# Optimization experiments

Measured on AMD Instinct MI355X. Metric: run time of the kernel, lower is better.

Reference implementation:

```python
import jax, jax.numpy as jnp
import numpy as np

EMBED = 1024
HEADS = 16
HEAD_DIM = EMBED // HEADS
MLP_HIDDEN = 4096


def _layernorm(x, g, b, eps=1e-5):
    mu = jnp.mean(x, axis=-1, keepdims=True)
    var = jnp.mean(jnp.square(x - mu), axis=-1, keepdims=True)
    return (x - mu) * jax.lax.rsqrt(var + eps) * g + b


def setup_inputs() -> dict:
    key = jax.random.key(0)
    ks = jax.random.split(key, 8)
    s = 0.02
    return {
        "x": jax.random.normal(ks[0], (8, 1024, EMBED), dtype=jnp.float32),
        "qkv_w": jax.random.normal(ks[1], (EMBED, 3 * EMBED), dtype=jnp.float32) * s,
        "qkv_b": jnp.zeros((3 * EMBED,), jnp.float32),
        "proj_w": jax.random.normal(ks[2], (EMBED, EMBED), dtype=jnp.float32) * s,
        "proj_b": jnp.zeros((EMBED,), jnp.float32),
        "fc1_w": jax.random.normal(ks[3], (EMBED, MLP_HIDDEN), dtype=jnp.float32) * s,
        "fc1_b": jnp.zeros((MLP_HIDDEN,), jnp.float32),
        "fc2_w": jax.random.normal(ks[4], (MLP_HIDDEN, EMBED), dtype=jnp.float32) * s,
        "fc2_b": jnp.zeros((EMBED,), jnp.float32),
        "ln1_g": jnp.ones((EMBED,), jnp.float32),
        "ln1_b": jnp.zeros((EMBED,), jnp.float32),
        "ln2_g": jnp.ones((EMBED,), jnp.float32),
        "ln2_b": jnp.zeros((EMBED,), jnp.float32),
    }


def reference(x, qkv_w, qkv_b, proj_w, proj_b, fc1_w, fc1_b, fc2_w, fc2_b,
              ln1_g, ln1_b, ln2_g, ln2_b):
    B, N, C = x.shape
    scale = HEAD_DIM ** -0.5

    # --- MHSA on pre-norm input ---
    h = _layernorm(x, ln1_g, ln1_b)
    qkv = h @ qkv_w + qkv_b                      # [B,N,3C]
    qkv = qkv.reshape(B, N, 3, HEADS, HEAD_DIM)
    q, k, v = (qkv[:, :, i].transpose(0, 2, 1, 3) for i in range(3))  # [B,H,N,d]
    attn = jnp.einsum('bhqd,bhkd->bhqk', q, k) * scale
    attn = jax.nn.softmax(attn, axis=-1)
    o = jnp.einsum('bhqk,bhkd->bhqd', attn, v)   # [B,H,N,d]
    o = o.transpose(0, 2, 1, 3).reshape(B, N, C)
    x = x + (o @ proj_w + proj_b)

    # --- MLP ---
    h2 = _layernorm(x, ln2_g, ln2_b)
    h2 = jax.nn.gelu(h2 @ fc1_w + fc1_b, approximate=False)
    x = x + (h2 @ fc2_w + fc2_b)
    return x
```

## Files before the change

### kernel.cpp

```cpp
#include <hip/hip_runtime.h>
#include <hip/hip_bf16.h>

typedef __bf16 bf16x8 __attribute__((ext_vector_type(8)));
typedef float  f32x4  __attribute__((ext_vector_type(4)));
typedef unsigned short u16;

static __device__ __forceinline__ u16 f2bf(float f) {
  union { float f; unsigned u; } v; v.f = f;
  unsigned r = v.u + 0x7fffu + ((v.u >> 16) & 1u);
  return (u16)(r >> 16);
}

static __device__ __forceinline__ void gld16(const void* g, void* l) {
  __builtin_amdgcn_global_load_lds(
      (const __attribute__((address_space(1))) unsigned int*)g,
      (__attribute__((address_space(3))) unsigned int*)l, 16, 0, 0);
}

#define SBAR() do { __builtin_amdgcn_sched_barrier(0); \
                    __builtin_amdgcn_s_barrier(); \
                    __builtin_amdgcn_sched_barrier(0); } while (0)

__global__ __launch_bounds__(256) void transpose_cast_k(
    const float* __restrict__ W, u16* __restrict__ Wt, int K, int N) {
  __shared__ float tile[32][33];
  const int t = threadIdx.x;
  const int n0 = blockIdx.x * 32, k0 = blockIdx.y * 32;
  const int r = t >> 3, c4 = (t & 7) * 4;
  const float4 v = *(const float4*)(W + (size_t)(k0 + r) * N + n0 + c4);
  tile[r][c4 + 0] = v.x; tile[r][c4 + 1] = v.y;
  tile[r][c4 + 2] = v.z; tile[r][c4 + 3] = v.w;
  __syncthreads();
  const int n = t >> 3, k4 = (t & 7) * 4;
  uint2 pk;
  pk.x = f2bf(tile[k4 + 0][n]) | ((unsigned)f2bf(tile[k4 + 1][n]) << 16);
  pk.y = f2bf(tile[k4 + 2][n]) | ((unsigned)f2bf(tile[k4 + 3][n]) << 16);
  *(uint2*)(Wt + (size_t)(n0 + n) * K + k0 + k4) = pk;
}

__global__ __launch_bounds__(256) void ln_cast_k(
    const float* __restrict__ x, const float* __restrict__ g,
    const float* __restrict__ b, u16* __restrict__ out) {
  __shared__ float red[2][4];
  const int t = threadIdx.x;
  const size_t row = blockIdx.x;
  const float4 v = *(const float4*)(x + row * 1024 + t * 4);
  float s = v.x + v.y + v.z + v.w;
  float ss = v.x * v.x + v.y * v.y + v.z * v.z + v.w * v.w;
  #pragma unroll
  for (int m = 1; m <= 32; m <<= 1) { s += __shfl_xor(s, m); ss += __shfl_xor(ss, m); }
  if ((t & 63) == 0) { red[0][t >> 6] = s; red[1][t >> 6] = ss; }
  __syncthreads();
  s  = red[0][0] + red[0][1] + red[0][2] + red[0][3];
  ss = red[1][0] + red[1][1] + red[1][2] + red[1][3];
  const float mu = s * (1.f / 1024.f);
  const float var = ss * (1.f / 1024.f) - mu * mu;
  const float rs = rsqrtf(var + 1e-5f);
  const float4 gv = *(const float4*)(g + t * 4);
  const float4 bv = *(const float4*)(b + t * 4);
  uint2 pk;
  pk.x = f2bf((v.x - mu) * rs * gv.x + bv.x) |
         ((unsigned)f2bf((v.y - mu) * rs * gv.y + bv.y) << 16);
  pk.y = f2bf((v.z - mu) * rs * gv.z + bv.z) |
         ((unsigned)f2bf((v.w - mu) * rs * gv.w + bv.w) << 16);
  *(uint2*)(out + row * 1024 + t * 4) = pk;
}

template <int EPI>
__global__ __launch_bounds__(512, 2) void gemm8_k(
    const u16* __restrict__ A, const u16* __restrict__ Bt,
    const float* __restrict__ bias, u16* __restrict__ Cb, float* __restrict__ Cf,
    const float* __restrict__ R, u16* __restrict__ vT, int M, int N, int K) {
  __shared__ u16 As[2][16384];
  __shared__ u16 Bs[2][16384];
  const int t = threadIdx.x;
  const int mt = M >> 8;
  const int tm = blockIdx.x % mt, tn = blockIdx.x / mt;
  const int lo = t & 15, hi = (t >> 4) & 3, wid = t >> 6;
  const int wm = wid >> 2, wn = wid & 3;
  const int NT = K >> 6;

  const int srow = t >> 3;
  const int sc = (t & 7) ^ (srow & 7);
  const u16* gA = A  + (size_t)(tm * 256) * K;
  const u16* gB = Bt + (size_t)(tn * 256) * K;
  auto stA = [&](int dd, int c, int T) {
    gld16(gA + (size_t)(c * 64 + srow) * K + (size_t)T * 64 + sc * 8,
          &As[dd][c * 4096 + t * 8]);
  };
  auto stB = [&](int dd, int c, int T) {
    gld16(gB + (size_t)(c * 64 + srow) * K + (size_t)T * 64 + sc * 8,
          &Bs[dd][c * 4096 + t * 8]);
  };

  const int xr = lo & 7;
  const int rowA = wm * 128 + lo;
  const int rowB = wn * 64 + lo;
#define RD_A(d, m, kk) (*(const bf16x8*)&As[d][(rowA + (m)*16)*64 + ((((kk)<<2)+hi)^xr)*8])
#define RD_B(d, n, kk) (*(const bf16x8*)&Bs[d][(rowB + (n)*16)*64 + ((((kk)<<2)+hi)^xr)*8])
#define MF(a, b, c) __builtin_amdgcn_mfma_f32_16x16x32_bf16(a, b, c, 0, 0, 0)

  f32x4 acc[8][4];
  #pragma unroll
  for (int i = 0; i < 8; ++i)
    #pragma unroll
    for (int j = 0; j < 4; ++j) acc[i][j] = (f32x4){0.f, 0.f, 0.f, 0.f};

  stA(0, 0, 0); stA(0, 1, 0); stA(0, 2, 0); stA(0, 3, 0);
  stB(0, 0, 0); stB(0, 1, 0); stB(0, 2, 0); stB(0, 3, 0);
  stB(1, 0, 1); stB(1, 1, 1); stB(1, 2, 1); stB(1, 3, 1);
  stA(1, 0, 1); stA(1, 2, 1);
  asm volatile("s_waitcnt vmcnt(6)" ::: "memory");
  SBAR();

  for (int T = 0; T < NT; ++T) {
    const int d = T & 1, dn = d ^ 1;
    bf16x8 b00 = RD_B(d,0,0), b01 = RD_B(d,0,1), b10 = RD_B(d,1,0), b11 = RD_B(d,1,1);
    bf16x8 b20 = RD_B(d,2,0), b21 = RD_B(d,2,1), b30 = RD_B(d,3,0), b31 = RD_B(d,3,1);
    bf16x8 a00 = RD_A(d,0,0), a01 = RD_A(d,0,1), a10 = RD_A(d,1,0), a11 = RD_A(d,1,1);
    if (T + 1 < NT) { stA(dn, 1, T + 1); stA(dn, 3, T + 1); }
    SBAR();
    __builtin_amdgcn_s_setprio(1);
    acc[0][0]=MF(a00,b00,acc[0][0]); acc[0][0]=MF(a01,b01,acc[0][0]);
    acc[0][1]=MF(a00,b10,acc[0][1]); acc[0][1]=MF(a01,b11,acc[0][1]);
    acc[0][2]=MF(a00,b20,acc[0][2]); acc[0][2]=MF(a01,b21,acc[0][2]);
    acc[0][3]=MF(a00,b30,acc[0][3]); acc[0][3]=MF(a01,b31,acc[0][3]);
    acc[1][0]=MF(a10,b00,acc[1][0]); acc[1][0]=MF(a11,b01,acc[1][0]);
    acc[1][1]=MF(a10,b10,acc[1][1]); acc[1][1]=MF(a11,b11,acc[1][1]);
    acc[1][2]=MF(a10,b20,acc[1][2]); acc[1][2]=MF(a11,b21,acc[1][2]);
    acc[1][3]=MF(a10,b30,acc[1][3]); acc[1][3]=MF(a11,b31,acc[1][3]);
    __builtin_amdgcn_s_setprio(0);
    SBAR();
    a00 = RD_A(d,2,0); a01 = RD_A(d,2,1); a10 = RD_A(d,3,0); a11 = RD_A(d,3,1);
    if (T + 2 < NT) { stB(d, 0, T + 2); stB(d, 1, T + 2); }
    SBAR();
    __builtin_amdgcn_s_setprio(1);
    acc[2][0]=MF(a00,b00,acc[2][0]); acc[2][0]=MF(a01,b01,acc[2][0]);
    acc[2][1]=MF(a00,b10,acc[2][1]); acc[2][1]=MF(a01,b11,acc[2][1]);
    acc[2][2]=MF(a00,b20,acc[2][2]); acc[2][2]=MF(a01,b21,acc[2][2]);
    acc[2][3]=MF(a00,b30,acc[2][3]); acc[2][3]=MF(a01,b31,acc[2][3]);
    acc[3][0]=MF(a10,b00,acc[3][0]); acc[3][0]=MF(a11,b01,acc[3][0]);
    acc[3][1]=MF(a10,b10,acc[3][1]); acc[3][1]=MF(a11,b11,acc[3][1]);
    acc[3][2]=MF(a10,b20,acc[3][2]); acc[3][2]=MF(a11,b21,acc[3][2]);
    acc[3][3]=MF(a10,b30,acc[3][3]); acc[3][3]=MF(a11,b31,acc[3][3]);
    __builtin_amdgcn_s_setprio(0);
    SBAR();
    a00 = RD_A(d,4,0); a01 = RD_A(d,4,1); a10 = RD_A(d,5,0); a11 = RD_A(d,5,1);
    if (T + 2 < NT) { stB(d, 2, T + 2); stB(d, 3, T + 2); }
    SBAR();
    __builtin_amdgcn_s_setprio(1);
    acc[4][0]=MF(a00,b00,acc[4][0]); acc[4][0]=MF(a01,b01,acc[4][0]);
    acc[4][1]=MF(a00,b10,acc[4][1]); acc[4][1]=MF(a01,b11,acc[4][1]);
    acc[4][2]=MF(a00,b20,acc[4][2]); acc[4][2]=MF(a01,b21,acc[4][2]);
    acc[4][3]=MF(a00,b30,acc[4][3]); acc[4][3]=MF(a01,b31,acc[4][3]);
    acc[5][0]=MF(a10,b00,acc[5][0]); acc[5][0]=MF(a11,b01,acc[5][0]);
    acc[5][1]=MF(a10,b10,acc[5][1]); acc[5][1]=MF(a11,b11,acc[5][1]);
    acc[5][2]=MF(a10,b20,acc[5][2]); acc[5][2]=MF(a11,b21,acc[5][2]);
    acc[5][3]=MF(a10,b30,acc[5][3]); acc[5][3]=MF(a11,b31,acc[5][3]);
    __builtin_amdgcn_s_setprio(0);
    SBAR();
    a00 = RD_A(d,6,0); a01 = RD_A(d,6,1); a10 = RD_A(d,7,0); a11 = RD_A(d,7,1);
    if (T + 2 < NT) { stA(d, 0, T + 2); stA(d, 2, T + 2); }
    SBAR();
    __builtin_amdgcn_s_setprio(1);
    acc[6][0]=MF(a00,b00,acc[6][0]); acc[6][0]=MF(a01,b01,acc[6][0]);
    acc[6][1]=MF(a00,b10,acc[6][1]); acc[6][1]=MF(a01,b11,acc[6][1]);
    acc[6][2]=MF(a00,b20,acc[6][2]); acc[6][2]=MF(a01,b21,acc[6][2]);
    acc[6][3]=MF(a00,b30,acc[6][3]); acc[6][3]=MF(a01,b31,acc[6][3]);
    acc[7][0]=MF(a10,b00,acc[7][0]); acc[7][0]=MF(a11,b01,acc[7][0]);
    acc[7][1]=MF(a10,b10,acc[7][1]); acc[7][1]=MF(a11,b11,acc[7][1]);
    acc[7][2]=MF(a10,b20,acc[7][2]); acc[7][2]=MF(a11,b21,acc[7][2]);
    acc[7][3]=MF(a10,b30,acc[7][3]); acc[7][3]=MF(a11,b31,acc[7][3]);
    __builtin_amdgcn_s_setprio(0);
    if (T < NT - 2)       { asm volatile("s_waitcnt vmcnt(6)" ::: "memory"); }
    else if (T == NT - 2) { asm volatile("s_waitcnt vmcnt(0)" ::: "memory"); }
    SBAR();
  }

  #pragma unroll
  for (int ni = 0; ni < 4; ++ni) {
    const int col = tn * 256 + wn * 64 + ni * 16 + lo;
    const float bv = bias[col];
    #pragma unroll
    for (int mi = 0; mi < 8; ++mi) {
      const int row0 = tm * 256 + wm * 128 + mi * 16 + hi * 4;
      const f32x4 v = acc[mi][ni];
      float vals[4];
      #pragma unroll
      for (int r = 0; r < 4; ++r) {
        float val = v[r] + bv;
        if (EPI == 1) val = 0.5f * val * (1.f + erff(val * 0.70710678118f));
        vals[r] = val;
      }
      if (EPI == 2) {
        #pragma unroll
        for (int r = 0; r < 4; ++r) {
          const size_t idx = (size_t)(row0 + r) * N + col;
          Cf[idx] = vals[r] + R[idx];
        }
      } else {
        #pragma unroll
        for (int r = 0; r < 4; ++r)
          Cb[(size_t)(row0 + r) * N + col] = f2bf(vals[r]);
        if (EPI == 3 && col >= 2048) {
          const int bb = row0 >> 10, n = row0 & 1023;
          const int hh = (col - 2048) >> 6, dd = col & 63;
          uint2 pk;
          pk.x = f2bf(vals[0]) | ((unsigned)f2bf(vals[1]) << 16);
          pk.y = f2bf(vals[2]) | ((unsigned)f2bf(vals[3]) << 16);
          *(uint2*)(vT + ((size_t)((bb * 16 + hh) * 64 + dd) << 10) + n) = pk;
        }
      }
    }
  }
#undef RD_A
#undef RD_B
#undef MF
}

__global__ __launch_bounds__(256, 2) void attn_k(
    const u16* __restrict__ qkv, const u16* __restrict__ vT, u16* __restrict__ o) {
  __shared__ u16 lK[64 * 64];
  __shared__ u16 lV[64 * 64];
  __shared__ u16 lP[64 * 72];
  const int t = threadIdx.x;
  const int lo = t & 15, hi = (t >> 4) & 3, w = t >> 6;
  const int qt = blockIdx.x & 15, bh = blockIdx.x >> 4;
  const int b = bh >> 4, h = bh & 15;
  const int q0 = qt * 64;
  const u16* Qb = qkv + (size_t)b * 1024 * 3072 + h * 64;
  const u16* Kb = Qb + 1024;
  const u16* Vt = vT + (size_t)bh * 64 * 1024;

  bf16x8 qf[2];
  {
    const size_t q = q0 + w * 16 + lo;
    qf[0] = *(const bf16x8*)(Qb + q * 3072 + hi * 8);
    qf[1] = *(const bf16x8*)(Qb + q * 3072 + 32 + hi * 8);
  }
  f32x4 oacc[4];
  #pragma unroll
  for (int i = 0; i < 4; ++i) oacc[i] = (f32x4){0.f, 0.f, 0.f, 0.f};
  float m = -1e30f, lsum = 0.f;
  const int srow = t >> 3, scol = (t & 7) * 8;

  for (int kv0 = 0; kv0 < 1024; kv0 += 64) {
    __syncthreads();
    #pragma unroll
    for (int j = 0; j < 2; ++j) {
      const int row = j * 32 + srow;
      gld16(Kb + (size_t)(kv0 + row) * 3072 + scol, &lK[(j * 256 + t) * 8]);
      gld16(Vt + (size_t)row * 1024 + kv0 + scol, &lV[(j * 256 + t) * 8]);
    }
    __syncthreads();

    f32x4 s[4];
    #pragma unroll
    for (int i = 0; i < 4; ++i) s[i] = (f32x4){0.f, 0.f, 0.f, 0.f};
    #pragma unroll
    for (int kk = 0; kk < 2; ++kk) {
      #pragma unroll
      for (int mi = 0; mi < 4; ++mi) {
        const bf16x8 kf = *(const bf16x8*)&lK[(mi * 16 + lo) * 64 + kk * 32 + hi * 8];
        s[mi] = __builtin_amdgcn_mfma_f32_16x16x32_bf16(kf, qf[kk], s[mi], 0, 0, 0);
      }
    }
    float sv[16];
    float tmax = -1e30f;
    #pragma unroll
    for (int mi = 0; mi < 4; ++mi)
      #pragma unroll
      for (int r = 0; r < 4; ++r) {
        const float xx = s[mi][r] * 0.125f;
        sv[mi * 4 + r] = xx;
        tmax = fmaxf(tmax, xx);
      }
    tmax = fmaxf(tmax, __shfl_xor(tmax, 16));
    tmax = fmaxf(tmax, __shfl_xor(tmax, 32));
    const float mnew = fmaxf(m, tmax);
    const float alpha = __expf(m - mnew);
    m = mnew;
    float p[16], ts = 0.f;
    #pragma unroll
    for (int i = 0; i < 16; ++i) { p[i] = __expf(sv[i] - mnew); ts += p[i]; }
    ts += __shfl_xor(ts, 16);
    ts += __shfl_xor(ts, 32);
    lsum = lsum * alpha + ts;
    #pragma unroll
    for (int mi = 0; mi < 4; ++mi) {
      uint2 pk;
      pk.x = f2bf(p[mi * 4 + 0]) | ((unsigned)f2bf(p[mi * 4 + 1]) << 16);
      pk.y = f2bf(p[mi * 4 + 2]) | ((unsigned)f2bf(p[mi * 4 + 3]) << 16);
      *(uint2*)&lP[(w * 16 + lo) * 72 + mi * 16 + hi * 4] = pk;
    }
    asm volatile("s_waitcnt lgkmcnt(0)" ::: "memory");
    float ar[4];
    #pragma unroll
    for (int r = 0; r < 4; ++r) ar[r] = __shfl(alpha, hi * 4 + r);
    #pragma unroll
    for (int ni = 0; ni < 4; ++ni)
      #pragma unroll
      for (int r = 0; r < 4; ++r) oacc[ni][r] *= ar[r];
    #pragma unroll
    for (int kk = 0; kk < 2; ++kk) {
      const bf16x8 pf = *(const bf16x8*)&lP[(w * 16 + lo) * 72 + kk * 32 + hi * 8];
      #pragma unroll
      for (int ni = 0; ni < 4; ++ni) {
        const bf16x8 vf = *(const bf16x8*)&lV[(ni * 16 + lo) * 64 + kk * 32 + hi * 8];
        oacc[ni] = __builtin_amdgcn_mfma_f32_16x16x32_bf16(pf, vf, oacc[ni], 0, 0, 0);
      }
    }
  }
  float lr[4];
  #pragma unroll
  for (int r = 0; r < 4; ++r) lr[r] = 1.f / __shfl(lsum, hi * 4 + r);
  #pragma unroll
  for (int ni = 0; ni < 4; ++ni) {
    const int d = ni * 16 + lo;
    #pragma unroll
    for (int r = 0; r < 4; ++r) {
      const int n = q0 + w * 16 + hi * 4 + r;
      o[((size_t)(b * 1024 + n) * 16 + h) * 64 + d] = f2bf(oacc[ni][r] * lr[r]);
    }
  }
}

extern "C" void kernel_launch(void* const* d_in, const int* in_sizes, int n_in,
                              void* d_out, int out_size, void* d_ws, size_t ws_size,
                              hipStream_t stream) {
  const float* x      = (const float*)d_in[0];
  const float* qkv_w  = (const float*)d_in[1];
  const float* qkv_b  = (const float*)d_in[2];
  const float* proj_w = (const float*)d_in[3];
  const float* proj_b = (const float*)d_in[4];
  const float* fc1_w  = (const float*)d_in[5];
  const float* fc1_b  = (const float*)d_in[6];
  const float* fc2_w  = (const float*)d_in[7];
  const float* fc2_b  = (const float*)d_in[8];
  const float* ln1_g  = (const float*)d_in[9];
  const float* ln1_b  = (const float*)d_in[10];
  const float* ln2_g  = (const float*)d_in[11];
  const float* ln2_b  = (const float*)d_in[12];
  float* out = (float*)d_out;
  char* ws = (char*)d_ws;
  u16* wqkvT = (u16*)(ws);
  u16* wprojT = (u16*)(ws + 6291456);
  u16* wfc1T = (u16*)(ws + 8388608);
  u16* wfc2T = (u16*)(ws + 16777216);
  u16* hbuf  = (u16*)(ws + 25165824);
  u16* qkvo  = (u16*)(ws + 41943040);
  u16* vT    = (u16*)(ws + 92274688);
  u16* fc1o  = qkvo;

  transpose_cast_k<<<dim3(96, 32),  256, 0, stream>>>(qkv_w,  wqkvT, 1024, 3072);
  transpose_cast_k<<<dim3(32, 32),  256, 0, stream>>>(proj_w, wprojT, 1024, 1024);
  transpose_cast_k<<<dim3(128, 32), 256, 0, stream>>>(fc1_w,  wfc1T, 1024, 4096);
  transpose_cast_k<<<dim3(32, 128), 256, 0, stream>>>(fc2_w,  wfc2T, 4096, 1024);
  ln_cast_k<<<8192, 256, 0, stream>>>(x, ln1_g, ln1_b, hbuf);
  gemm8_k<3><<<32 * 12, 512, 0, stream>>>(hbuf, wqkvT, qkv_b, qkvo, nullptr, nullptr, vT, 8192, 3072, 1024);
  attn_k<<<2048, 256, 0, stream>>>(qkvo, vT, hbuf);
  gemm8_k<2><<<32 * 4, 512, 0, stream>>>(hbuf, wprojT, proj_b, nullptr, out, x, nullptr, 8192, 1024, 1024);
  ln_cast_k<<<8192, 256, 0, stream>>>(out, ln2_g, ln2_b, hbuf);
  gemm8_k<1><<<32 * 16, 512, 0, stream>>>(hbuf, wfc1T, fc1_b, fc1o, nullptr, nullptr, nullptr, 8192, 4096, 1024);
  gemm8_k<2><<<32 * 4, 512, 0, stream>>>(fc1o, wfc2T, fc2_b, nullptr, out, out, nullptr, 8192, 1024, 4096);
}
```

Before: 461.3 us.

## Add 256x128 GEMM tile variant and XCD-aware block swizzle for small GEMMs

Templates the GEMM on the number of N-warps, adding a 256x128 tile variant with its own LDS staging schedule. The QKV, proj and fc2 GEMMs now use it, which doubles their block count so the 256-CU device is better filled (proj/fc2 previously launched only 128 blocks). It also remaps block indices so consecutive blocks land on the same XCD, and interleaves the MFMA order. The smaller tile lowers arithmetic intensity per block and raises traffic for the A operand.

```diff
diff --git a/kernel.cpp b/kernel.cpp
--- a/kernel.cpp
+++ b/kernel.cpp
@@ -66,24 +66,28 @@
   *(uint2*)(out + row * 1024 + t * 4) = pk;
 }
 
-template <int EPI>
+template <int EPI, int WN>
 __global__ __launch_bounds__(512, 2) void gemm8_k(
     const u16* __restrict__ A, const u16* __restrict__ Bt,
     const float* __restrict__ bias, u16* __restrict__ Cb, float* __restrict__ Cf,
     const float* __restrict__ R, u16* __restrict__ vT, int M, int N, int K) {
+  constexpr int MR = 2 * WN;
+  constexpr int BN = 64 * WN;
   __shared__ u16 As[2][16384];
-  __shared__ u16 Bs[2][16384];
+  __shared__ u16 Bs[2][WN * 4096];
   const int t = threadIdx.x;
-  const int mt = M >> 8;
-  const int tm = blockIdx.x % mt, tn = blockIdx.x / mt;
+  const int nt = N / BN;
+  const int q = gridDim.x >> 3;
+  const int swz = (blockIdx.x & 7) * q + (blockIdx.x >> 3);
+  const int tn = swz % nt, tm = swz / nt;
   const int lo = t & 15, hi = (t >> 4) & 3, wid = t >> 6;
-  const int wm = wid >> 2, wn = wid & 3;
+  const int wm = wid / WN, wn = wid & (WN - 1);
   const int NT = K >> 6;
 
   const int srow = t >> 3;
   const int sc = (t & 7) ^ (srow & 7);
   const u16* gA = A  + (size_t)(tm * 256) * K;
-  const u16* gB = Bt + (size_t)(tn * 256) * K;
+  const u16* gB = Bt + (size_t)(tn * BN) * K;
   auto stA = [&](int dd, int c, int T) {
     gld16(gA + (size_t)(c * 64 + srow) * K + (size_t)T * 64 + sc * 8,
           &As[dd][c * 4096 + t * 8]);
@@ -94,96 +98,86 @@
   };
 
   const int xr = lo & 7;
-  const int rowA = wm * 128 + lo;
+  const int rowA = wm * (MR * 16) + lo;
   const int rowB = wn * 64 + lo;
 #define RD_A(d, m, kk) (*(const bf16x8*)&As[d][(rowA + (m)*16)*64 + ((((kk)<<2)+hi)^xr)*8])
 #define RD_B(d, n, kk) (*(const bf16x8*)&Bs[d][(rowB + (n)*16)*64 + ((((kk)<<2)+hi)^xr)*8])
 #define MF(a, b, c) __builtin_amdgcn_mfma_f32_16x16x32_bf16(a, b, c, 0, 0, 0)
 
-  f32x4 acc[8][4];
-  #pragma unroll
-  for (int i = 0; i < 8; ++i)
+  f32x4 acc[MR][4];
+  #pragma unroll
+  for (int i = 0; i < MR; ++i)
     #pragma unroll
     for (int j = 0; j < 4; ++j) acc[i][j] = (f32x4){0.f, 0.f, 0.f, 0.f};
 
-  stA(0, 0, 0); stA(0, 1, 0); stA(0, 2, 0); stA(0, 3, 0);
-  stB(0, 0, 0); stB(0, 1, 0); stB(0, 2, 0); stB(0, 3, 0);
-  stB(1, 0, 1); stB(1, 1, 1); stB(1, 2, 1); stB(1, 3, 1);
-  stA(1, 0, 1); stA(1, 2, 1);
-  asm volatile("s_waitcnt vmcnt(6)" ::: "memory");
-  SBAR();
-
-  for (int T = 0; T < NT; ++T) {
-    const int d = T & 1, dn = d ^ 1;
-    bf16x8 b00 = RD_B(d,0,0), b01 = RD_B(d,0,1), b10 = RD_B(d,1,0), b11 = RD_B(d,1,1);
-    bf16x8 b20 = RD_B(d,2,0), b21 = RD_B(d,2,1), b30 = RD_B(d,3,0), b31 = RD_B(d,3,1);
-    bf16x8 a00 = RD_A(d,0,0), a01 = RD_A(d,0,1), a10 = RD_A(d,1,0), a11 = RD_A(d,1,1);
-    if (T + 1 < NT) { stA(dn, 1, T + 1); stA(dn, 3, T + 1); }
+#define PH16(d, M0, M1, STAGES, WAITS) do { \
+    bf16x8 a0 = RD_A(d, M0, 0), a1 = RD_A(d, M0, 1); \
+    bf16x8 a2 = RD_A(d, M1, 0), a3 = RD_A(d, M1, 1); \
+    STAGES; SBAR(); __builtin_amdgcn_s_setprio(1); \
+    acc[M0][0]=MF(a0,b00,acc[M0][0]); acc[M0][1]=MF(a0,b10,acc[M0][1]); \
+    acc[M0][2]=MF(a0,b20,acc[M0][2]); acc[M0][3]=MF(a0,b30,acc[M0][3]); \
+    acc[M1][0]=MF(a2,b00,acc[M1][0]); acc[M1][1]=MF(a2,b10,acc[M1][1]); \
+    acc[M1][2]=MF(a2,b20,acc[M1][2]); acc[M1][3]=MF(a2,b30,acc[M1][3]); \
+    acc[M0][0]=MF(a1,b01,acc[M0][0]); acc[M0][1]=MF(a1,b11,acc[M0][1]); \
+    acc[M0][2]=MF(a1,b21,acc[M0][2]); acc[M0][3]=MF(a1,b31,acc[M0][3]); \
+    acc[M1][0]=MF(a3,b01,acc[M1][0]); acc[M1][1]=MF(a3,b11,acc[M1][1]); \
+    acc[M1][2]=MF(a3,b21,acc[M1][2]); acc[M1][3]=MF(a3,b31,acc[M1][3]); \
+    __builtin_amdgcn_s_setprio(0); WAITS; SBAR(); } while (0)
+
+#define PH8(d, M0, STAGES, WAITS) do { \
+    bf16x8 a0 = RD_A(d, M0, 0), a1 = RD_A(d, M0, 1); \
+    STAGES; SBAR(); __builtin_amdgcn_s_setprio(1); \
+    acc[M0][0]=MF(a0,b00,acc[M0][0]); acc[M0][1]=MF(a0,b10,acc[M0][1]); \
+    acc[M0][2]=MF(a0,b20,acc[M0][2]); acc[M0][3]=MF(a0,b30,acc[M0][3]); \
+    acc[M0][0]=MF(a1,b01,acc[M0][0]); acc[M0][1]=MF(a1,b11,acc[M0][1]); \
+    acc[M0][2]=MF(a1,b21,acc[M0][2]); acc[M0][3]=MF(a1,b31,acc[M0][3]); \
+    __builtin_amdgcn_s_setprio(0); WAITS; SBAR(); } while (0)
+
+  if constexpr (WN == 4) {
+    stA(0, 0, 0); stA(0, 1, 0); stA(0, 2, 0); stA(0, 3, 0);
+    stB(0, 0, 0); stB(0, 1, 0); stB(0, 2, 0); stB(0, 3, 0);
+    stB(1, 0, 1); stB(1, 1, 1); stB(1, 2, 1); stB(1, 3, 1);
+    stA(1, 0, 1); stA(1, 2, 1);
+    asm volatile("s_waitcnt vmcnt(6)" ::: "memory");
     SBAR();
-    __builtin_amdgcn_s_setprio(1);
-    acc[0][0]=MF(a00,b00,acc[0][0]); acc[0][0]=MF(a01,b01,acc[0][0]);
-    acc[0][1]=MF(a00,b10,acc[0][1]); acc[0][1]=MF(a01,b11,acc[0][1]);
-    acc[0][2]=MF(a00,b20,acc[0][2]); acc[0][2]=MF(a01,b21,acc[0][2]);
-    acc[0][3]=MF(a00,b30,acc[0][3]); acc[0][3]=MF(a01,b31,acc[0][3]);
-    acc[1][0]=MF(a10,b00,acc[1][0]); acc[1][0]=MF(a11,b01,acc[1][0]);
-    acc[1][1]=MF(a10,b10,acc[1][1]); acc[1][1]=MF(a11,b11,acc[1][1]);
-    acc[1][2]=MF(a10,b20,acc[1][2]); acc[1][2]=MF(a11,b21,acc[1][2]);
-    acc[1][3]=MF(a10,b30,acc[1][3]); acc[1][3]=MF(a11,b31,acc[1][3]);
-    __builtin_amdgcn_s_setprio(0);
+    for (int T = 0; T < NT; ++T) {
+      const int d = T & 1, dn = d ^ 1;
+      bf16x8 b00 = RD_B(d,0,0), b01 = RD_B(d,0,1), b10 = RD_B(d,1,0), b11 = RD_B(d,1,1);
+      bf16x8 b20 = RD_B(d,2,0), b21 = RD_B(d,2,1), b30 = RD_B(d,3,0), b31 = RD_B(d,3,1);
+      PH16(d, 0, 1, { if (T + 1 < NT) { stA(dn, 1, T + 1); stA(dn, 3, T + 1); } }, );
+      PH16(d, 2, 3, { if (T + 2 < NT) { stB(d, 0, T + 2); stB(d, 1, T + 2); } }, );
+      PH16(d, 4, 5, { if (T + 2 < NT) { stB(d, 2, T + 2); stB(d, 3, T + 2); } }, );
+      PH16(d, 6, 7, { if (T + 2 < NT) { stA(d, 0, T + 2); stA(d, 2, T + 2); } },
+           { if (T < NT - 2)       { asm volatile("s_waitcnt vmcnt(6)" ::: "memory"); }
+             else if (T == NT - 2) { asm volatile("s_waitcnt vmcnt(0)" ::: "memory"); } });
+    }
+  } else {
+    stA(0, 0, 0); stA(0, 1, 0); stA(0, 2, 0); stA(0, 3, 0);
+    stB(0, 0, 0); stB(0, 1, 0);
+    stB(1, 0, 1); stB(1, 1, 1);
+    asm volatile("s_waitcnt vmcnt(2)" ::: "memory");
     SBAR();
-    a00 = RD_A(d,2,0); a01 = RD_A(d,2,1); a10 = RD_A(d,3,0); a11 = RD_A(d,3,1);
-    if (T + 2 < NT) { stB(d, 0, T + 2); stB(d, 1, T + 2); }
-    SBAR();
-    __builtin_amdgcn_s_setprio(1);
-    acc[2][0]=MF(a00,b00,acc[2][0]); acc[2][0]=MF(a01,b01,acc[2][0]);
-    acc[2][1]=MF(a00,b10,acc[2][1]); acc[2][1]=MF(a01,b11,acc[2][1]);
-    acc[2][2]=MF(a00,b20,acc[2][2]); acc[2][2]=MF(a01,b21,acc[2][2]);
-    acc[2][3]=MF(a00,b30,acc[2][3]); acc[2][3]=MF(a01,b31,acc[2][3]);
-    acc[3][0]=MF(a10,b00,acc[3][0]); acc[3][0]=MF(a11,b01,acc[3][0]);
-    acc[3][1]=MF(a10,b10,acc[3][1]); acc[3][1]=MF(a11,b11,acc[3][1]);
-    acc[3][2]=MF(a10,b20,acc[3][2]); acc[3][2]=MF(a11,b21,acc[3][2]);
-    acc[3][3]=MF(a10,b30,acc[3][3]); acc[3][3]=MF(a11,b31,acc[3][3]);
-    __builtin_amdgcn_s_setprio(0);
-    SBAR();
-    a00 = RD_A(d,4,0); a01 = RD_A(d,4,1); a10 = RD_A(d,5,0); a11 = RD_A(d,5,1);
-    if (T + 2 < NT) { stB(d, 2, T + 2); stB(d, 3, T + 2); }
-    SBAR();
-    __builtin_amdgcn_s_setprio(1);
-    acc[4][0]=MF(a00,b00,acc[4][0]); acc[4][0]=MF(a01,b01,acc[4][0]);
-    acc[4][1]=MF(a00,b10,acc[4][1]); acc[4][1]=MF(a01,b11,acc[4][1]);
-    acc[4][2]=MF(a00,b20,acc[4][2]); acc[4][2]=MF(a01,b21,acc[4][2]);
-    acc[4][3]=MF(a00,b30,acc[4][3]); acc[4][3]=MF(a01,b31,acc[4][3]);
-    acc[5][0]=MF(a10,b00,acc[5][0]); acc[5][0]=MF(a11,b01,acc[5][0]);
-    acc[5][1]=MF(a10,b10,acc[5][1]); acc[5][1]=MF(a11,b11,acc[5][1]);
-    acc[5][2]=MF(a10,b20,acc[5][2]); acc[5][2]=MF(a11,b21,acc[5][2]);
-    acc[5][3]=MF(a10,b30,acc[5][3]); acc[5][3]=MF(a11,b31,acc[5][3]);
-    __builtin_amdgcn_s_setprio(0);
-    SBAR();
-    a00 = RD_A(d,6,0); a01 = RD_A(d,6,1); a10 = RD_A(d,7,0); a11 = RD_A(d,7,1);
-    if (T + 2 < NT) { stA(d, 0, T + 2); stA(d, 2, T + 2); }
-    SBAR();
-    __builtin_amdgcn_s_setprio(1);
-    acc[6][0]=MF(a00,b00,acc[6][0]); acc[6][0]=MF(a01,b01,acc[6][0]);
-    acc[6][1]=MF(a00,b10,acc[6][1]); acc[6][1]=MF(a01,b11,acc[6][1]);
-    acc[6][2]=MF(a00,b20,acc[6][2]); acc[6][2]=MF(a01,b21,acc[6][2]);
-    acc[6][3]=MF(a00,b30,acc[6][3]); acc[6][3]=MF(a01,b31,acc[6][3]);
-    acc[7][0]=MF(a10,b00,acc[7][0]); acc[7][0]=MF(a11,b01,acc[7][0]);
-    acc[7][1]=MF(a10,b10,acc[7][1]); acc[7][1]=MF(a11,b11,acc[7][1]);
-    acc[7][2]=MF(a10,b20,acc[7][2]); acc[7][2]=MF(a11,b21,acc[7][2]);
-    acc[7][3]=MF(a10,b30,acc[7][3]); acc[7][3]=MF(a11,b31,acc[7][3]);
-    __builtin_amdgcn_s_setprio(0);
-    if (T < NT - 2)       { asm volatile("s_waitcnt vmcnt(6)" ::: "memory"); }
-    else if (T == NT - 2) { asm volatile("s_waitcnt vmcnt(0)" ::: "memory"); }
-    SBAR();
+    for (int T = 0; T < NT; ++T) {
+      const int d = T & 1, dn = d ^ 1;
+      bf16x8 b00 = RD_B(d,0,0), b01 = RD_B(d,0,1), b10 = RD_B(d,1,0), b11 = RD_B(d,1,1);
+      bf16x8 b20 = RD_B(d,2,0), b21 = RD_B(d,2,1), b30 = RD_B(d,3,0), b31 = RD_B(d,3,1);
+      PH8(d, 0, { if (T + 1 < NT) { stA(dn, 0, T + 1); stA(dn, 1, T + 1);
+                                    stA(dn, 2, T + 1); stA(dn, 3, T + 1); } }, );
+      PH8(d, 1, { if (T + 2 < NT) { stB(d, 0, T + 2); stB(d, 1, T + 2); } }, );
+      PH8(d, 2, , );
+      PH8(d, 3, ,
+          { if (T < NT - 2)       { asm volatile("s_waitcnt vmcnt(2)" ::: "memory"); }
+            else if (T == NT - 2) { asm volatile("s_waitcnt vmcnt(0)" ::: "memory"); } });
+    }
   }
 
   #pragma unroll
   for (int ni = 0; ni < 4; ++ni) {
-    const int col = tn * 256 + wn * 64 + ni * 16 + lo;
+    const int col = tn * BN + wn * 64 + ni * 16 + lo;
     const float bv = bias[col];
     #pragma unroll
-    for (int mi = 0; mi < 8; ++mi) {
-      const int row0 = tm * 256 + wm * 128 + mi * 16 + hi * 4;
+    for (int mi = 0; mi < MR; ++mi) {
+      const int row0 = tm * 256 + wm * (MR * 16) + mi * 16 + hi * 4;
       const f32x4 v = acc[mi][ni];
       float vals[4];
       #pragma unroll
@@ -216,6 +210,8 @@
 #undef RD_A
 #undef RD_B
 #undef MF
+#undef PH16
+#undef PH8
 }
 
 __global__ __launch_bounds__(256, 2) void attn_k(
@@ -357,10 +353,10 @@
   transpose_cast_k<<<dim3(128, 32), 256, 0, stream>>>(fc1_w,  wfc1T, 1024, 4096);
   transpose_cast_k<<<dim3(32, 128), 256, 0, stream>>>(fc2_w,  wfc2T, 4096, 1024);
   ln_cast_k<<<8192, 256, 0, stream>>>(x, ln1_g, ln1_b, hbuf);
-  gemm8_k<3><<<32 * 12, 512, 0, stream>>>(hbuf, wqkvT, qkv_b, qkvo, nullptr, nullptr, vT, 8192, 3072, 1024);
+  gemm8_k<3, 2><<<768, 512, 0, stream>>>(hbuf, wqkvT, qkv_b, qkvo, nullptr, nullptr, vT, 8192, 3072, 1024);
   attn_k<<<2048, 256, 0, stream>>>(qkvo, vT, hbuf);
-  gemm8_k<2><<<32 * 4, 512, 0, stream>>>(hbuf, wprojT, proj_b, nullptr, out, x, nullptr, 8192, 1024, 1024);
+  gemm8_k<2, 2><<<256, 512, 0, stream>>>(hbuf, wprojT, proj_b, nullptr, out, x, nullptr, 8192, 1024, 1024);
   ln_cast_k<<<8192, 256, 0, stream>>>(out, ln2_g, ln2_b, hbuf);
-  gemm8_k<1><<<32 * 16, 512, 0, stream>>>(hbuf, wfc1T, fc1_b, fc1o, nullptr, nullptr, nullptr, 8192, 4096, 1024);
-  gemm8_k<2><<<32 * 4, 512, 0, stream>>>(fc1o, wfc2T, fc2_b, nullptr, out, out, nullptr, 8192, 1024, 4096);
-}
+  gemm8_k<1, 4><<<512, 512, 0, stream>>>(hbuf, wfc1T, fc1_b, fc1o, nullptr, nullptr, nullptr, 8192, 4096, 1024);
+  gemm8_k<2, 2><<<256, 512, 0, stream>>>(fc1o, wfc2T, fc2_b, nullptr, out, out, nullptr, 8192, 1024, 4096);
+}
```

Result: faster. 427.2 us (-7.4%).
